# Kernel tuning notes

Measured on AMD Instinct MI355X. Metric: run time of the kernel, lower is better.

Reference implementation:

```python
import jax, jax.numpy as jnp
import numpy as np
from jax import lax

FS = 44100.0
B, T = 8, 22050
N_CH, LG, LH, M = 31, 2048, 512, 12
F32 = np.float32


def _bp_fir(f1, f2, K, fs):
    # windowed-sinc bandpass FIR, peak-normalized
    t = np.arange(K) - (K - 1) / 2.0
    lp = lambda fc: 2.0 * fc / fs * np.sinc(2.0 * fc / fs * t)
    h = (lp(f2) - lp(f1)) * np.hamming(K)
    return (h / np.abs(np.fft.rfft(h)).max()).astype(F32)


def _gammatone_fir(fs, K, flow, fhigh, n_ch):
    # 4th-order gammatone impulse responses, 1-ERB spaced fc, peak-normalized
    erb = lambda f: 21.4 * np.log10(4.37 * f / 1000.0 + 1.0)
    ierb = lambda e: (10.0 ** (e / 21.4) - 1.0) * 1000.0 / 4.37
    fc = ierb(np.linspace(erb(flow), erb(fhigh), n_ch))
    t = np.arange(K) / fs
    bw = 1.019 * 24.7 * (4.37 * fc / 1000.0 + 1.0)
    g = t[None] ** 3 * np.exp(-2 * np.pi * bw[:, None] * t[None]) * np.cos(2 * np.pi * fc[:, None] * t[None])
    g = g / np.abs(np.fft.rfft(g, axis=1)).max(axis=1, keepdims=True)
    return g.astype(F32)


def setup_inputs():
    key = jax.random.key(0)
    x = jax.random.normal(key, (B, T), dtype=jnp.float32) * 0.01
    return {
        "x": x,
        "hp_fir": jnp.asarray(_bp_fir(50.0, 16000.0, LH, FS)),   # headphone/outer ear
        "me_fir": jnp.asarray(_bp_fir(450.0, 8500.0, LH, FS)),   # middle ear
        "gt_fir": jnp.asarray(_gammatone_fir(FS, LG, 80.0, 8000.0, N_CH)),
    }


def _conv_causal(x, h):
    # x: [B, Cin, T]; h: [Cout, Cin, K]. Kernel flipped so this is true FIR convolution, causal padding.
    K = h.shape[-1]
    return lax.conv_general_dilated(x, h[:, :, ::-1], (1,), [(K - 1, 0)],
                                    dimension_numbers=("NCH", "OIH", "NCH"))


def _forward(x, hp_fir, me_fir, gt_fir):
    # Stage 0a/0b: headphone + middle-ear FIR
    y = _conv_causal(x[:, None, :], hp_fir[None, None, :])
    y = _conv_causal(y, me_fir[None, None, :])
    # Stage 1: gammatone filterbank -> [B, N, T]
    y = _conv_causal(y, gt_fir[:, None, :])
    bsz, nch, _ = y.shape

    # Stage 2: IHC envelope (breebaart2001): halfwave rectify + 5 cascaded one-pole LP @ 2 kHz
    hw = jnp.maximum(y, 0.0)
    a_lp = jnp.float32(np.exp(-2.0 * np.pi * 2000.0 / FS))

    def ihc_step(s, xt):  # s: [5, B, N], xt: [B, N]
        s0 = a_lp * s[0] + (1.0 - a_lp) * xt
        s1 = a_lp * s[1] + (1.0 - a_lp) * s0
        s2 = a_lp * s[2] + (1.0 - a_lp) * s1
        s3 = a_lp * s[3] + (1.0 - a_lp) * s2
        s4 = a_lp * s[4] + (1.0 - a_lp) * s3
        return jnp.stack([s0, s1, s2, s3, s4]), s4

    _, env = lax.scan(ihc_step, jnp.zeros((5, bsz, nch), jnp.float32), jnp.moveaxis(hw, -1, 0))  # env: [T,B,N]

    # Stage 3: adaptation loops (5 loops, osses2021 limit=5)
    minlvl = jnp.float32(1e-5)
    taus = np.array([0.005, 0.05, 0.129, 0.253, 0.5], F32)
    a1 = jnp.asarray(np.exp(-1.0 / (FS * taus)).astype(F32))
    b0 = 1.0 - a1
    init = np.float32(1e-5) ** (2.0 ** -np.arange(1, 6, dtype=F32))  # sqrt chain of minlvl
    limit = np.float32(5.0)
    maxv = (1.0 - init ** 2) * limit - 1.0
    factor = jnp.asarray(2.0 * maxv)
    expfac = jnp.asarray(-2.0 / maxv)
    offset = jnp.asarray(maxv - 1.0)
    state0 = jnp.broadcast_to(jnp.asarray(init)[:, None, None], (5, bsz, nch)).astype(jnp.float32)

    def adapt_step(state, xt):  # state: [5, B, N]
        tmp = jnp.maximum(xt, minlvl)
        new = []
        for j in range(5):
            tmp = tmp / state[j]
            limited = factor[j] / (1.0 + jnp.exp(expfac[j] * (tmp - 1.0))) - offset[j]
            tmp = jnp.where(tmp > 1.0, limited, tmp)
            new.append(a1[j] * state[j] + b0[j] * tmp)
        return jnp.stack(new), tmp

    _, ad = lax.scan(adapt_step, state0, env)  # ad: [T, B, N]
    corr = np.float32(1e-5) ** np.float32(2.0 ** -5)
    ad = (ad - corr) * (100.0 / (1.0 - corr))  # model units (MU)

    # Stage 4: modulation filterbank (jepsen2008-style): M complex one-pole resonators (Q=2),
    # real part for mfc<=10 Hz, 1/sqrt(2)-attenuated envelope above.
    mfc = jnp.asarray(np.array([2.5, 5.0, 10.0, 16.7, 27.8, 46.3, 77.2,
                                128.6, 214.3, 357.2, 595.4, 992.3], F32))
    r = jnp.exp(-jnp.pi * (mfc / 2.0) / FS)
    pole = (r * jnp.exp(1j * 2.0 * jnp.pi * mfc / FS)).astype(jnp.complex64)
    b0m = (1.0 - r).astype(jnp.complex64)
    att = jnp.float32(1.0 / np.sqrt(2.0))
    lowband = mfc <= 10.0

    def mod_step(s, xt):  # s: [B, N, M] complex, xt: [B, N]
        s = pole * s + b0m * xt[..., None]
        out = jnp.where(lowband, s.real, att * jnp.sqrt(s.real ** 2 + s.imag ** 2 + 1e-12))
        return s, out

    _, mo = lax.scan(mod_step, jnp.zeros((bsz, nch, M), jnp.complex64), ad)  # mo: [T, B, N, M]
    return jnp.moveaxis(mo, 0, -1)  # [B, N, M, T]


def reference(x, hp_fir, me_fir, gt_fir):
    return _forward(x, hp_fir, me_fir, gt_fir)
```

## Files before the change

### kernel.cpp

```cpp
#include <hip/hip_runtime.h>
#include <math.h>

#define FS_   44100.0
#define B_    8
#define T_    22050
#define NCH   31
#define LG    2048
#define LH    512
#define MM    12
#define BN    248

#define H1LEN 1023

#define C2T   512
#define C2THR 128

#define IHCK  128

#define MODL  441
#define MODC  50

#define NBLK  62
#define TQ    5520
#define ADP   22052

#define OFF_H1    0
#define OFF_G5    1024
#define OFF_X1    1280
#define OFF_HW    177696
#define OFF_AD    OFF_HW
#define OFF_ENV   (OFF_HW + 5468896)
#define OFF_SEND  (OFF_ENV + 5475840)
#define OFF_SINIT (OFF_SEND + 297600)

struct ScanP {
  float a1[5], b0[5], factor[5], efl2[5], offset[5], init[5], rinit[5];
  float minlvl, corr, scale;
};
struct ModP {
  float pre[12], pim[12], pb0[12], pLre[12], pLim[12];
  float att;
};

typedef float f32x4_t __attribute__((ext_vector_type(4)));

__global__ void k_h1(const float* __restrict__ hp, const float* __restrict__ me,
                     float* __restrict__ h1) {
  int k = blockIdx.x * blockDim.x + threadIdx.x;
  if (k >= H1LEN) return;
  int j0 = max(0, k - (LH - 1));
  int j1 = min(LH - 1, k);
  float acc = 0.f;
  for (int j = j0; j <= j1; ++j) acc += hp[j] * me[k - j];
  h1[k] = acc;
}

__global__ void k_g5(float l2a, float c5, float* __restrict__ g5) {
  int k = threadIdx.x;
  float kf = (float)k;
  float binom = (kf + 1.f) * (kf + 2.f) * (kf + 3.f) * (kf + 4.f) * (1.0f / 24.0f);
  g5[k] = c5 * binom * exp2f(kf * l2a);
}

__global__ void k_conv1(const float* __restrict__ x, const float* __restrict__ h1,
                        float* __restrict__ x1) {
  __shared__ float xs[256 + 1022];
  __shared__ float hs[H1LEN];
  int b = blockIdx.y;
  int t0 = blockIdx.x * 256;
  const float* xb = x + b * T_;
  for (int i = threadIdx.x; i < 1278; i += 256) {
    int g = t0 - 1022 + i;
    xs[i] = (g >= 0 && g < T_) ? xb[g] : 0.f;
  }
  for (int i = threadIdx.x; i < H1LEN; i += 256) hs[i] = h1[i];
  __syncthreads();
  int t = t0 + threadIdx.x;
  if (t >= T_) return;
  float acc = 0.f;
  for (int k = 0; k < H1LEN; ++k) acc = fmaf(hs[k], xs[threadIdx.x + 1022 - k], acc);
  x1[b * T_ + t] = acc;
}

__global__ __launch_bounds__(C2THR) void k_conv2(const float* __restrict__ x1,
                                                 const float* __restrict__ gt,
                                                 float* __restrict__ hw) {
  const int H = LG - 1;
  __shared__ __align__(16) float xs[C2T + LG];
  int n = blockIdx.y % NCH, b = blockIdx.y / NCH;
  int t0 = blockIdx.x * C2T;
  const float* xb = x1 + b * T_;
  for (int i = threadIdx.x; i < C2T + LG; i += C2THR) {
    int g = t0 - H + i;
    xs[i] = (g >= 0 && g < T_) ? xb[g] : 0.f;
  }
  __syncthreads();
  const float* gtn = gt + n * LG;
  int base = threadIdx.x * 4;
  float a0 = 0.f, a1 = 0.f, a2 = 0.f, a3 = 0.f;
  float4 hi = *(const float4*)&xs[base + H + 1];
  for (int k4 = 0; k4 < LG / 4; ++k4) {
    int k = k4 * 4;
    float4 lo = *(const float4*)&xs[base + H - 3 - k];
    float h0 = gtn[k + 0], h1v = gtn[k + 1], h2 = gtn[k + 2], h3 = gtn[k + 3];
    a0 = fmaf(h0,  lo.w, a0); a1 = fmaf(h0,  hi.x, a1); a2 = fmaf(h0,  hi.y, a2); a3 = fmaf(h0,  hi.z, a3);
    a0 = fmaf(h1v, lo.z, a0); a1 = fmaf(h1v, lo.w, a1); a2 = fmaf(h1v, hi.x, a2); a3 = fmaf(h1v, hi.y, a3);
    a0 = fmaf(h2,  lo.y, a0); a1 = fmaf(h2,  lo.z, a1); a2 = fmaf(h2,  lo.w, a2); a3 = fmaf(h2,  hi.x, a3);
    a0 = fmaf(h3,  lo.x, a0); a1 = fmaf(h3,  lo.y, a1); a2 = fmaf(h3,  lo.z, a2); a3 = fmaf(h3,  lo.w, a3);
    hi = lo;
  }
  float* o = hw + (size_t)(b * NCH + n) * T_;
  int t = t0 + base;
  if (t + 0 < T_) o[t + 0] = fmaxf(a0, 0.f);
  if (t + 1 < T_) o[t + 1] = fmaxf(a1, 0.f);
  if (t + 2 < T_) o[t + 2] = fmaxf(a2, 0.f);
  if (t + 3 < T_) o[t + 3] = fmaxf(a3, 0.f);
}

__global__ __launch_bounds__(C2THR) void k_ihc(const float* __restrict__ hw,
                                               const float* __restrict__ g5,
                                               float* __restrict__ env) {
  const int H = IHCK - 1;
  __shared__ __align__(16) float xs[C2T + IHCK];
  int bn = blockIdx.y;
  int t0 = blockIdx.x * C2T;
  const float* xb = hw + (size_t)bn * T_;
  for (int i = threadIdx.x; i < C2T + IHCK; i += C2THR) {
    int g = t0 - H + i;
    xs[i] = (g >= 0 && g < T_) ? xb[g] : 0.f;
  }
  __syncthreads();
  int base = threadIdx.x * 4;
  float a0 = 0.f, a1 = 0.f, a2 = 0.f, a3 = 0.f;
  float4 hi = *(const float4*)&xs[base + H + 1];
  for (int k4 = 0; k4 < IHCK / 4; ++k4) {
    int k = k4 * 4;
    float4 lo = *(const float4*)&xs[base + H - 3 - k];
    float h0 = g5[k + 0], h1v = g5[k + 1], h2 = g5[k + 2], h3 = g5[k + 3];
    a0 = fmaf(h0,  lo.w, a0); a1 = fmaf(h0,  hi.x, a1); a2 = fmaf(h0,  hi.y, a2); a3 = fmaf(h0,  hi.z, a3);
    a0 = fmaf(h1v, lo.z, a0); a1 = fmaf(h1v, lo.w, a1); a2 = fmaf(h1v, hi.x, a2); a3 = fmaf(h1v, hi.y, a3);
    a0 = fmaf(h2,  lo.y, a0); a1 = fmaf(h2,  lo.z, a1); a2 = fmaf(h2,  lo.w, a2); a3 = fmaf(h2,  hi.x, a3);
    a0 = fmaf(h3,  lo.x, a0); a1 = fmaf(h3,  lo.y, a1); a2 = fmaf(h3,  lo.z, a2); a3 = fmaf(h3,  lo.w, a3);
    hi = lo;
  }
  int t = t0 + base;
  if (t < T_) {
    int blk = bn >> 2, s = bn & 3, tq = t >> 2;
    float4* o4 = (float4*)(env + ((size_t)(blk * TQ + tq) * 4 + s) * 4);
    *o4 = make_float4(a0, a1, a2, a3);
  }
}

#define GLD0(DST, PTR)  asm volatile("global_load_dwordx4 %0, %1, off"            : "=v"(DST) : "v"(PTR) : "memory")
#define GLD(DST, PTR, OFFB) \
  asm volatile("global_load_dwordx4 %0, %1, off offset:" #OFFB : "=v"(DST) : "v"(PTR) : "memory")
#define VMWAIT(N) do { asm volatile("s_waitcnt vmcnt(" #N ")" ::: "memory"); \
                       __builtin_amdgcn_sched_barrier(0); } while (0)

__global__ __launch_bounds__(64, 1) void k_scan(const float* __restrict__ env,
                                                float* __restrict__ ad, ScanP p) {
  const int lane = threadIdx.x;
  const int row = lane >> 4, q = lane & 15;
  const int seq = blockIdx.x * 4 + row;
  const bool is4 = (q == 4);
  const float* eb = env + (size_t)blockIdx.x * TQ * 16 + row * 4;
  float* o = ad + (size_t)seq * ADP;

#define SEL5(A) (q==0 ? (A)[0] : q==1 ? (A)[1] : q==2 ? (A)[2] : q==3 ? (A)[3] : (A)[4])
  const float A1  = SEL5(p.a1),   B0  = SEL5(p.b0), FAC = SEL5(p.factor);
  const float EF  = SEL5(p.efl2), NEF = -EF,        NOFF = -SEL5(p.offset);
  float st = SEL5(p.init);
  float r  = SEL5(p.rinit);
#undef SEL5
  const float SC = p.scale, NCS = -p.corr * p.scale, ML = p.minlvl;

  float a1st = A1 * st;
  float tmp = 0.f;
  float o0 = 0.f, o1 = 0.f, o2 = 0.f, o3 = 0.f;

#define BODY(EV)                                                              \
    float evc = fmaxf((EV), ML);                                              \
    float tin = __int_as_float(__builtin_amdgcn_update_dpp(                   \
        __float_as_int(evc), __float_as_int(tmp), 0x111, 0xF, 0xF, false));   \
    float v   = tin * r;                                                      \
    float ex  = __builtin_amdgcn_exp2f(fmaf(EF, v, NEF));                     \
    float lim = fmaf(FAC, __builtin_amdgcn_rcpf(1.0f + ex), NOFF);            \
    tmp = fminf(v, lim);

#define STEP_FILL(EV, K)                                                      \
  { BODY(EV)                                                                  \
    float nst = fmaf(B0, tmp, a1st);                                          \
    st = ((K) >= q) ? nst : st;                                               \
    a1st = A1 * st;                                                           \
    r  = __builtin_amdgcn_rcpf(st); }

#define STEP(EV, OSLOT)                                                       \
  { BODY(EV)                                                                  \
    st = fmaf(B0, tmp, a1st);                                                 \
    a1st = A1 * st;                                                           \
    r  = __builtin_amdgcn_rcpf(st);                                           \
    OSLOT = fmaf(tmp, SC, NCS); }

  f32x4_t bF, b0, b1, b2, b3, b4, b5, b6, b7;
  GLD0(bF, eb);
  GLD(b0, eb, 64);   GLD(b1, eb, 128);  GLD(b2, eb, 192);  GLD(b3, eb, 256);
  GLD(b4, eb, 320);  GLD(b5, eb, 384);  GLD(b6, eb, 448);  GLD(b7, eb, 512);
  VMWAIT(0);

  STEP_FILL(bF.x, 0) STEP_FILL(bF.y, 1) STEP_FILL(bF.z, 2) STEP_FILL(bF.w, 3)

  const float* pld = eb + 9 * 16;
  float* po = o;

#define SUBSTEP(BUF, FOFF, BOFF)                                              \
    VMWAIT(14);                                                               \
    STEP(BUF.x, o0) STEP(BUF.y, o1) STEP(BUF.z, o2) STEP(BUF.w, o3)           \
    if (is4) *(float4*)(po + FOFF) = make_float4(o0, o1, o2, o3);             \
    GLD(BUF, pld, BOFF);

  for (int j = 0; j < 689; ++j) {
    SUBSTEP(b0,  0,   0)
    SUBSTEP(b1,  4,  64)
    SUBSTEP(b2,  8, 128)
    SUBSTEP(b3, 12, 192)
    SUBSTEP(b4, 16, 256)
    SUBSTEP(b5, 20, 320)
    SUBSTEP(b6, 24, 384)
    SUBSTEP(b7, 28, 448)
    pld += 8 * 16;
    po  += 32;
  }
#undef SUBSTEP

  STEP(0.f, o0) STEP(0.f, o1)
  if (is4) *(float4*)(o + 22048) = make_float4(o0, o1, o2, o3);
#undef STEP
#undef STEP_FILL
#undef BODY
}

__global__ void k_modA(const float* __restrict__ ad, float2* __restrict__ send, ModP mp) {
  int id = blockIdx.x * 256 + threadIdx.x;
  if (id >= MODC * BN * MM) return;
  int m = id % MM, bn = (id / MM) % BN, c = id / (MM * BN);
  const float* a = ad + (size_t)bn * ADP + c * MODL;
  float pre = mp.pre[m], pim = mp.pim[m], b0 = mp.pb0[m];
  float sre = 0.f, sim = 0.f;
  for (int i = 0; i < MODL; ++i) {
    float xv = a[i];
    float nre = fmaf(pre, sre, fmaf(-pim, sim, b0 * xv));
    sim = fmaf(pre, sim, pim * sre);
    sre = nre;
  }
  send[id] = make_float2(sre, sim);
}

__global__ void k_modB(const float2* __restrict__ send, float2* __restrict__ sinit, ModP mp) {
  int id = blockIdx.x * blockDim.x + threadIdx.x;
  if (id >= BN * MM) return;
  int m = id % MM;
  float pLre = mp.pLre[m], pLim = mp.pLim[m];
  float Sre = 0.f, Sim = 0.f;
  for (int c = 0; c < MODC; ++c) {
    int idx = c * BN * MM + id;
    sinit[idx] = make_float2(Sre, Sim);
    float2 se = send[idx];
    float nre = pLre * Sre - pLim * Sim + se.x;
    Sim = pLre * Sim + pLim * Sre + se.y;
    Sre = nre;
  }
}

__global__ void k_modC(const float* __restrict__ ad, const float2* __restrict__ sinit,
                       float* __restrict__ out, ModP mp) {
  int id = blockIdx.x * 256 + threadIdx.x;
  if (id >= MODC * BN * MM) return;
  int m = id % MM, bn = (id / MM) % BN, c = id / (MM * BN);
  const float* a = ad + (size_t)bn * ADP + c * MODL;
  float* o = out + ((size_t)bn * MM + m) * T_ + c * MODL;
  float2 s0 = sinit[id];
  float sre = s0.x, sim = s0.y;
  float pre = mp.pre[m], pim = mp.pim[m], b0 = mp.pb0[m], att = mp.att;
  bool low = (m < 3);
  for (int i = 0; i < MODL; ++i) {
    float xv = a[i];
    float nre = fmaf(pre, sre, fmaf(-pim, sim, b0 * xv));
    sim = fmaf(pre, sim, pim * sre);
    sre = nre;
    float mag = att * sqrtf(fmaf(sre, sre, fmaf(sim, sim, 1e-12f)));
    o[i] = low ? sre : mag;
  }
}

extern "C" void kernel_launch(void* const* d_in, const int* in_sizes, int n_in,
                              void* d_out, int out_size, void* d_ws, size_t ws_size,
                              hipStream_t stream) {
  const float* x  = (const float*)d_in[0];
  const float* hp = (const float*)d_in[1];
  const float* me = (const float*)d_in[2];
  const float* gt = (const float*)d_in[3];
  float* ws  = (float*)d_ws;
  float* out = (float*)d_out;

  ScanP sp;
  const double taus[5] = {0.005, 0.05, 0.129, 0.253, 0.5};
  for (int j = 0; j < 5; ++j) {
    double a1 = exp(-1.0 / (FS_ * taus[j]));
    double init = pow(1e-5, pow(2.0, -(double)(j + 1)));
    double maxv = (1.0 - init * init) * 5.0 - 1.0;
    sp.a1[j] = (float)a1;
    sp.b0[j] = (float)(1.0 - a1);
    sp.factor[j] = (float)(2.0 * maxv);
    sp.efl2[j] = (float)(-2.0 / maxv * 1.4426950408889634);
    sp.offset[j] = (float)(maxv - 1.0);
    sp.init[j] = (float)init;
    sp.rinit[j] = (float)(1.0 / init);
  }
  sp.minlvl = 1e-5f;
  double corr = pow(1e-5, pow(2.0, -5.0));
  sp.corr = (float)corr;
  sp.scale = (float)(100.0 / (1.0 - corr));

  ModP mp;
  const double mfc[12] = {2.5, 5.0, 10.0, 16.7, 27.8, 46.3, 77.2, 128.6, 214.3, 357.2, 595.4, 992.3};
  for (int m = 0; m < 12; ++m) {
    double r = exp(-M_PI * (mfc[m] / 2.0) / FS_);
    double th = 2.0 * M_PI * mfc[m] / FS_;
    mp.pre[m] = (float)(r * cos(th));
    mp.pim[m] = (float)(r * sin(th));
    mp.pb0[m] = (float)(1.0 - r);
    double rL = pow(r, (double)MODL);
    mp.pLre[m] = (float)(rL * cos((double)MODL * th));
    mp.pLim[m] = (float)(rL * sin((double)MODL * th));
  }
  mp.att = (float)(1.0 / sqrt(2.0));

  double alp = exp(-2.0 * M_PI * 2000.0 / FS_);
  float l2a = (float)(log(alp) * 1.4426950408889634);
  float c5  = (float)pow(1.0 - alp, 5.0);

  float* h1  = ws + OFF_H1;
  float* g5  = ws + OFF_G5;
  float* x1  = ws + OFF_X1;
  float* hw  = ws + OFF_HW;
  float* env = ws + OFF_ENV;
  float* ad  = ws + OFF_AD;
  float2* send  = (float2*)(ws + OFF_SEND);
  float2* sinit = (float2*)(ws + OFF_SINIT);

  k_h1<<<dim3(2), dim3(512), 0, stream>>>(hp, me, h1);
  k_g5<<<dim3(1), dim3(128), 0, stream>>>(l2a, c5, g5);
  k_conv1<<<dim3(87, B_), dim3(256), 0, stream>>>(x, h1, x1);
  k_conv2<<<dim3((T_ + C2T - 1) / C2T, BN), dim3(C2THR), 0, stream>>>(x1, gt, hw);
  k_ihc<<<dim3((T_ + C2T - 1) / C2T, BN), dim3(C2THR), 0, stream>>>(hw, g5, env);
  k_scan<<<dim3(NBLK), dim3(64), 0, stream>>>(env, ad, sp);
  int nmod = MODC * BN * MM;
  k_modA<<<dim3((nmod + 255) / 256), dim3(256), 0, stream>>>(ad, send, mp);
  k_modB<<<dim3((BN * MM + 255) / 256), dim3(256), 0, stream>>>(send, sinit, mp);
  k_modC<<<dim3((nmod + 255) / 256), dim3(256), 0, stream>>>(ad, sinit, out, mp);
}
```

Baseline: 1.766 ms.

## Stage modulation outputs through shared-memory tile for coalesced global stores

The final modulation kernel now buffers each thread's 63-sample chunk of outputs in a shared-memory tile, then writes rows cooperatively so consecutive lanes store consecutive time samples. This replaces the old pattern where each thread wrote its own strided output row, which gave uncoalesced stores. The grid becomes 2D over (channel-bank groups, time chunks). Separately, conv1 reads filter taps directly from global/constant-cached memory instead of copying them to shared memory. The shared tile is about 63 KB per block, which limits occupancy and adds barriers.

```diff
diff --git a/kernel.cpp b/kernel.cpp
--- a/kernel.cpp
+++ b/kernel.cpp
@@ -19,6 +19,7 @@
 
 #define MODL  441
 #define MODC  50
+#define MCT   63
 
 #define NBLK  62
 #define TQ    5520
@@ -65,7 +66,6 @@
 __global__ void k_conv1(const float* __restrict__ x, const float* __restrict__ h1,
                         float* __restrict__ x1) {
   __shared__ float xs[256 + 1022];
-  __shared__ float hs[H1LEN];
   int b = blockIdx.y;
   int t0 = blockIdx.x * 256;
   const float* xb = x + b * T_;
@@ -73,12 +73,11 @@
     int g = t0 - 1022 + i;
     xs[i] = (g >= 0 && g < T_) ? xb[g] : 0.f;
   }
-  for (int i = threadIdx.x; i < H1LEN; i += 256) hs[i] = h1[i];
   __syncthreads();
   int t = t0 + threadIdx.x;
   if (t >= T_) return;
   float acc = 0.f;
-  for (int k = 0; k < H1LEN; ++k) acc = fmaf(hs[k], xs[threadIdx.x + 1022 - k], acc);
+  for (int k = 0; k < H1LEN; ++k) acc = fmaf(h1[k], xs[threadIdx.x + 1022 - k], acc);
   x1[b * T_ + t] = acc;
 }
 
@@ -271,24 +270,41 @@
   }
 }
 
-__global__ void k_modC(const float* __restrict__ ad, const float2* __restrict__ sinit,
-                       float* __restrict__ out, ModP mp) {
-  int id = blockIdx.x * 256 + threadIdx.x;
-  if (id >= MODC * BN * MM) return;
-  int m = id % MM, bn = (id / MM) % BN, c = id / (MM * BN);
+__global__ __launch_bounds__(256) void k_modC(const float* __restrict__ ad,
+                                              const float2* __restrict__ sinit,
+                                              float* __restrict__ out, ModP mp) {
+  __shared__ float tile[256][MCT];
+  const int tid = threadIdx.x;
+  const int c = blockIdx.y;
+  const int idc = blockIdx.x * 256 + tid;
+  const bool act = idc < BN * MM;
+  const int idcc = act ? idc : 0;
+  const int m = idcc % MM, bn = idcc / MM;
   const float* a = ad + (size_t)bn * ADP + c * MODL;
-  float* o = out + ((size_t)bn * MM + m) * T_ + c * MODL;
-  float2 s0 = sinit[id];
+  float2 s0 = sinit[c * BN * MM + idcc];
   float sre = s0.x, sim = s0.y;
-  float pre = mp.pre[m], pim = mp.pim[m], b0 = mp.pb0[m], att = mp.att;
-  bool low = (m < 3);
-  for (int i = 0; i < MODL; ++i) {
-    float xv = a[i];
-    float nre = fmaf(pre, sre, fmaf(-pim, sim, b0 * xv));
-    sim = fmaf(pre, sim, pim * sre);
-    sre = nre;
-    float mag = att * sqrtf(fmaf(sre, sre, fmaf(sim, sim, 1e-12f)));
-    o[i] = low ? sre : mag;
+  const float pre = mp.pre[m], pim = mp.pim[m], b0 = mp.pb0[m], att = mp.att;
+  const bool low = (m < 3);
+  const int wv = tid >> 6, ln = tid & 63;
+  for (int tb = 0; tb < 7; ++tb) {
+    for (int i = 0; i < MCT; ++i) {
+      float xv = a[tb * MCT + i];
+      float nre = fmaf(pre, sre, fmaf(-pim, sim, b0 * xv));
+      sim = fmaf(pre, sim, pim * sre);
+      sre = nre;
+      float mag = att * sqrtf(fmaf(sre, sre, fmaf(sim, sim, 1e-12f)));
+      tile[tid][i] = low ? sre : mag;
+    }
+    __syncthreads();
+    if (ln < MCT) {
+      for (int rr = 0; rr < 64; ++rr) {
+        int rowi = (wv << 6) + rr;
+        int gid = blockIdx.x * 256 + rowi;
+        if (gid < BN * MM)
+          out[(size_t)gid * T_ + c * MODL + tb * MCT + ln] = tile[rowi][ln];
+      }
+    }
+    __syncthreads();
   }
 }
 
@@ -357,5 +373,5 @@
   int nmod = MODC * BN * MM;
   k_modA<<<dim3((nmod + 255) / 256), dim3(256), 0, stream>>>(ad, send, mp);
   k_modB<<<dim3((BN * MM + 255) / 256), dim3(256), 0, stream>>>(send, sinit, mp);
-  k_modC<<<dim3((nmod + 255) / 256), dim3(256), 0, stream>>>(ad, sinit, out, mp);
-}
+  k_modC<<<dim3((BN * MM + 255) / 256, MODC), dim3(256), 0, stream>>>(ad, sinit, out, mp);
+}
```

Measured after the change: 1.694 ms. -4.1%, faster.
